# Kernel optimization log

Hardware: AMD Instinct MI355X
Metric: run time of the kernel (lower is better)

The kernel has to match this reference:

```python
import jax, jax.numpy as jnp
import numpy as np

D_MODEL = 1024
NUM_HEADS = 16
HEAD_DIM = D_MODEL // NUM_HEADS


def setup_inputs() -> dict:
    key = jax.random.key(0)
    k1, k2, k3 = jax.random.split(key, 3)
    x = jax.random.normal(k1, (2, 2048, D_MODEL), dtype=jnp.float32)
    # trunc_normal init approximated by clipped normal with same std
    std_qkv = np.sqrt(2.0 / (D_MODEL + 3 * D_MODEL)).astype(np.float32)
    std_o = np.sqrt(2.0 / (D_MODEL + D_MODEL)).astype(np.float32)
    w_qkv = jnp.clip(jax.random.normal(k2, (3 * D_MODEL, D_MODEL), dtype=jnp.float32) * std_qkv,
                     -3 * std_qkv, 3 * std_qkv)
    w_o = jnp.clip(jax.random.normal(k3, (D_MODEL, D_MODEL), dtype=jnp.float32) * std_o,
                   -3 * std_o, 3 * std_o)
    return {"x": x, "w_qkv": w_qkv, "w_o": w_o}


def reference(x, w_qkv, w_o):
    b, s, d = x.shape
    h, hd = NUM_HEADS, HEAD_DIM
    # QKV projection: weight is [d_out, d_in]
    qkv = jnp.einsum('od,bsd->bso', w_qkv, x)  # [b, s, 3d]
    q, k, v = jnp.split(qkv, 3, axis=-1)
    # [b, s, d] -> [b, h, s, hd]
    def to_heads(t):
        return t.reshape(b, s, h, hd).transpose(0, 2, 1, 3)
    q_mh, k_mh, v_mh = to_heads(q), to_heads(k), to_heads(v)
    scale = 1.0 / jnp.sqrt(jnp.asarray(hd, dtype=x.dtype))
    scores = jnp.einsum('bhmd,bhnd->bhmn', q_mh, k_mh) * scale  # [b,h,s,s]
    causal = jnp.tril(jnp.ones((s, s), dtype=bool))
    scores = jnp.where(causal, scores, -jnp.inf)
    attn = jax.nn.softmax(scores, axis=-1)
    out = jnp.einsum('bhmn,bhnd->bhmd', attn, v_mh)  # [b,h,s,hd]
    out = out.transpose(0, 2, 1, 3).reshape(b, s, d)
    return jnp.einsum('od,bsd->bso', w_o, out)
```

## Files before the change

kernel.cpp:

```cpp
#include <hip/hip_runtime.h>

constexpr int SEQ = 2048;
constexpr int DM = 1024;
constexpr int NH = 16;
constexpr int BATCH = 2;
constexpr int MTOT = BATCH * SEQ;

typedef __bf16 bf16x8 __attribute__((ext_vector_type(8)));
typedef __bf16 bf16x4 __attribute__((ext_vector_type(4)));
typedef float f32x4 __attribute__((ext_vector_type(4)));

#define MFMA16(a, b, c) __builtin_amdgcn_mfma_f32_16x16x32_bf16((a), (b), (c), 0, 0, 0)

__device__ __forceinline__ void async_copy16(const void* g, void* l) {
  __builtin_amdgcn_global_load_lds((const __attribute__((address_space(1))) void*)g,
                                   (__attribute__((address_space(3))) void*)l, 16, 0, 0);
}

__global__ void sentinel_fill(float* out, int n) {
  int i = blockIdx.x * blockDim.x + threadIdx.x;
  for (; i < n; i += gridDim.x * blockDim.x) out[i] = 0.25f;
}

__global__ __launch_bounds__(256) void cvt_all(const float* __restrict__ x,
                                               const float* __restrict__ wq,
                                               const float* __restrict__ wo,
                                               __bf16* __restrict__ xb,
                                               __bf16* __restrict__ wqb,
                                               __bf16* __restrict__ wob) {
  const long i = (long)(blockIdx.x * 256 + threadIdx.x) * 8;
  const float* src;
  __bf16* dst;
  long off;
  if (i < 4194304) { src = x; dst = xb; off = i; }
  else if (i < 7340032) { src = wq; dst = wqb; off = i - 4194304; }
  else { src = wo; dst = wob; off = i - 7340032; }
  f32x4 lo = *(const f32x4*)(src + off);
  f32x4 hi = *(const f32x4*)(src + off + 4);
  bf16x8 r;
#pragma unroll
  for (int j = 0; j < 4; ++j) { r[j] = (__bf16)lo[j]; r[4 + j] = (__bf16)hi[j]; }
  *(bf16x8*)(dst + off) = r;
}

template <typename OutT>
__global__ __launch_bounds__(256) void gemm_bt(const __bf16* __restrict__ A,
                                               const __bf16* __restrict__ B,
                                               OutT* __restrict__ C,
                                               int M, int N, int K, int lda,
                                               float nanSig) {
  __shared__ alignas(16) __bf16 As[128 * 32];
  __shared__ alignas(16) __bf16 Bs[128 * 32];
  const int tid = threadIdx.x;
  const int lane = tid & 63;
  const int wave = tid >> 6;
  const int lr = lane & 15;
  const int quad = lane >> 4;
  const int wm = (wave >> 1) * 64;
  const int wn = (wave & 1) * 64;
  const int m0 = blockIdx.y * 128;
  const int n0 = blockIdx.x * 128;

  const int ra = tid >> 2;
  const int ca = (tid & 3) * 8;
  const __bf16* gA0 = A + (long)(m0 + ra) * lda + ca;
  const __bf16* gA1 = A + (long)(m0 + 64 + ra) * lda + ca;
  const __bf16* gB0 = B + (long)(n0 + ra) * K + ca;
  const __bf16* gB1 = B + (long)(n0 + 64 + ra) * K + ca;
  __bf16* lA0 = &As[wave * 512];
  __bf16* lA1 = &As[2048 + wave * 512];
  __bf16* lB0 = &Bs[wave * 512];
  __bf16* lB1 = &Bs[2048 + wave * 512];

  f32x4 acc[4][4];
#pragma unroll
  for (int i = 0; i < 4; ++i)
#pragma unroll
    for (int j = 0; j < 4; ++j) acc[i][j] = (f32x4){0.f, 0.f, 0.f, 0.f};

  for (int k0 = 0; k0 < K; k0 += 32) {
    async_copy16(gA0 + k0, lA0);
    async_copy16(gA1 + k0, lA1);
    async_copy16(gB0 + k0, lB0);
    async_copy16(gB1 + k0, lB1);
    __builtin_amdgcn_s_waitcnt(0);
    __syncthreads();
    bf16x8 af[4], bfr[4];
#pragma unroll
    for (int i = 0; i < 4; ++i) af[i] = *(const bf16x8*)&As[(wm + i * 16 + lr) * 32 + quad * 8];
#pragma unroll
    for (int j = 0; j < 4; ++j) bfr[j] = *(const bf16x8*)&Bs[(wn + j * 16 + lr) * 32 + quad * 8];
#pragma unroll
    for (int i = 0; i < 4; ++i)
#pragma unroll
      for (int j = 0; j < 4; ++j) acc[i][j] = MFMA16(af[i], bfr[j], acc[i][j]);
    __syncthreads();
  }

#pragma unroll
  for (int i = 0; i < 4; ++i) {
    const int row = m0 + wm + i * 16 + quad * 4;
#pragma unroll
    for (int j = 0; j < 4; ++j) {
      const int col = n0 + wn + j * 16 + lr;
#pragma unroll
      for (int r = 0; r < 4; ++r) {
        float v = acc[i][j][r];
        if (!(v == v)) v = nanSig;
        C[(long)(row + r) * N + col] = (OutT)v;
      }
    }
  }
}

template <int F32>
__device__ __forceinline__ bf16x8 load_cvt8(const void* base, long off) {
  if constexpr (F32) {
    const float* p = (const float*)base + off;
    f32x4 lo = *(const f32x4*)p;
    f32x4 hi = *(const f32x4*)(p + 4);
    bf16x8 r;
#pragma unroll
    for (int j = 0; j < 4; ++j) { r[j] = (__bf16)lo[j]; r[4 + j] = (__bf16)hi[j]; }
    return r;
  } else {
    return *(const bf16x8*)((const __bf16*)base + off);
  }
}

template <int AF32, int BF32, typename OutT>
__global__ __launch_bounds__(256) void gemm_nt(const void* __restrict__ Av,
                                               const void* __restrict__ Bv,
                                               OutT* __restrict__ C,
                                               int M, int N, int K, int lda,
                                               float nanSig) {
  __shared__ alignas(16) __bf16 As[128 * 32];
  __shared__ alignas(16) __bf16 Bs[128 * 32];
  const int tid = threadIdx.x;
  const int lane = tid & 63;
  const int wave = tid >> 6;
  const int lr = lane & 15;
  const int quad = lane >> 4;
  const int wm = (wave >> 1) * 64;
  const int wn = (wave & 1) * 64;
  const int m0 = blockIdx.y * 128;
  const int n0 = blockIdx.x * 128;

  const int r0 = tid >> 2;
  const int r1 = 64 + (tid >> 2);
  const int cc = (tid & 3) * 8;
  const long aBase0 = (long)(m0 + r0) * lda + cc;
  const long aBase1 = (long)(m0 + r1) * lda + cc;
  const long bBase0 = (long)(n0 + r0) * K + cc;
  const long bBase1 = (long)(n0 + r1) * K + cc;
  __bf16* lA0 = &As[r0 * 32 + cc];
  __bf16* lA1 = &As[r1 * 32 + cc];
  __bf16* lB0 = &Bs[r0 * 32 + cc];
  __bf16* lB1 = &Bs[r1 * 32 + cc];

  f32x4 acc[4][4];
#pragma unroll
  for (int i = 0; i < 4; ++i)
#pragma unroll
    for (int j = 0; j < 4; ++j) acc[i][j] = (f32x4){0.f, 0.f, 0.f, 0.f};

  for (int k0 = 0; k0 < K; k0 += 32) {
    bf16x8 va0 = load_cvt8<AF32>(Av, aBase0 + k0);
    bf16x8 va1 = load_cvt8<AF32>(Av, aBase1 + k0);
    bf16x8 vb0 = load_cvt8<BF32>(Bv, bBase0 + k0);
    bf16x8 vb1 = load_cvt8<BF32>(Bv, bBase1 + k0);
    __syncthreads();
    *(bf16x8*)lA0 = va0;
    *(bf16x8*)lA1 = va1;
    *(bf16x8*)lB0 = vb0;
    *(bf16x8*)lB1 = vb1;
    __syncthreads();
    bf16x8 af[4], bfr[4];
#pragma unroll
    for (int i = 0; i < 4; ++i) af[i] = *(const bf16x8*)&As[(wm + i * 16 + lr) * 32 + quad * 8];
#pragma unroll
    for (int j = 0; j < 4; ++j) bfr[j] = *(const bf16x8*)&Bs[(wn + j * 16 + lr) * 32 + quad * 8];
#pragma unroll
    for (int i = 0; i < 4; ++i)
#pragma unroll
      for (int j = 0; j < 4; ++j) acc[i][j] = MFMA16(af[i], bfr[j], acc[i][j]);
  }

#pragma unroll
  for (int i = 0; i < 4; ++i) {
    const int row = m0 + wm + i * 16 + quad * 4;
#pragma unroll
    for (int j = 0; j < 4; ++j) {
      const int col = n0 + wn + j * 16 + lr;
#pragma unroll
      for (int r = 0; r < 4; ++r) {
        float v = acc[i][j][r];
        if (!(v == v)) v = nanSig;
        C[(long)(row + r) * N + col] = (OutT)v;
      }
    }
  }
}

__global__ __launch_bounds__(256, 2) void attn_fwd(__bf16* __restrict__ qkv) {
  const int pi = blockIdx.x;
  const int h = blockIdx.y;
  const int b = blockIdx.z;
  const int q0A = pi * 64;
  const int q0B = (31 - pi) * 64;
  const int tid = threadIdx.x;
  const int lane = tid & 63;
  const int wave = tid >> 6;
  const int lr = lane & 15;
  const int quad = lane >> 4;
  const int wq = wave * 16;

  __shared__ alignas(16) __bf16 Ks[64 * 72];
  __shared__ alignas(16) __bf16 Vt[64 * 72];
  __shared__ alignas(16) __bf16 Pq[128 * 72];

  __bf16* pqw = &Pq[wave * 32 * 72];
  const long base = (long)b * SEQ * 3072;
  const int qi[2] = {q0A + wq + lr, q0B + wq + lr};

  bf16x8 b_q[2][2];
#pragma unroll
  for (int qg = 0; qg < 2; ++qg) {
    const long rowoff = base + (long)qi[qg] * 3072 + h * 64;
    b_q[qg][0] = *(const bf16x8*)(qkv + rowoff + quad * 8);
    b_q[qg][1] = *(const bf16x8*)(qkv + rowoff + 32 + quad * 8);
  }

  const float NEGS = -30000.f;
  const float SC = 0.18033688f;
  float m_i[2] = {NEGS, NEGS}, l_i[2] = {0.f, 0.f};
  f32x4 o_acc[2][4];
#pragma unroll
  for (int qg = 0; qg < 2; ++qg)
#pragma unroll
    for (int dt = 0; dt < 4; ++dt) o_acc[qg][dt] = (f32x4){0.f, 0.f, 0.f, 0.f};

  const int r_ = tid >> 3;
  const int col_ = (tid & 7) * 8;
  const int l8 = tid & 7;
  const int sw = (l8 & 3) << 3;
  const bool oddr = (tid >> 3) & 1;
  const int jb = oddr ? 4 : 0;

  const int T = 32 - pi;

  bf16x8 kreg[2], vreg[2];
  {
    const long ro = base + (long)r_ * 3072 + h * 64 + col_;
    kreg[0] = *(const bf16x8*)(qkv + ro + 1024);
    kreg[1] = *(const bf16x8*)(qkv + ro + (long)32 * 3072 + 1024);
    vreg[0] = *(const bf16x8*)(qkv + ro + 2048);
    vreg[1] = *(const bf16x8*)(qkv + ro + (long)32 * 3072 + 2048);
  }

  for (int t = 0; t < T; ++t) {
    const int kv0 = t * 64;
    __syncthreads();
    *(bf16x8*)&Ks[r_ * 72 + col_] = kreg[0];
    *(bf16x8*)&Ks[(r_ + 32) * 72 + col_] = kreg[1];
#pragma unroll
    for (int c = 0; c < 2; ++c) {
      const int r = r_ + c * 32;
      const int rr = (r & ~1) ^ sw;
      int vd[4], od[4];
      __builtin_memcpy(vd, &vreg[c], 16);
#pragma unroll
      for (int i = 0; i < 4; ++i) od[i] = __shfl_xor(vd[i], 8);
#pragma unroll
      for (int i = 0; i < 4; ++i) {
        const int j = jb + i;
        const int a = vd[j >> 1], bb = od[j >> 1];
        const int lo = oddr ? bb : a;
        const int hi = oddr ? a : bb;
        const int pair = (j & 1) ? (int)(((unsigned)lo >> 16) | (hi & 0xffff0000))
                                 : (int)((lo & 0xffff) | (hi << 16));
        *(int*)&Vt[(col_ + j) * 72 + rr] = pair;
      }
    }
    __syncthreads();

    if (t + 1 < T) {
      const long ro = base + ((long)(t + 1) * 64 + r_) * 3072 + h * 64 + col_;
      kreg[0] = *(const bf16x8*)(qkv + ro + 1024);
      kreg[1] = *(const bf16x8*)(qkv + ro + (long)32 * 3072 + 1024);
      vreg[0] = *(const bf16x8*)(qkv + ro + 2048);
      vreg[1] = *(const bf16x8*)(qkv + ro + (long)32 * 3072 + 2048);
    }

    const bool actA = (kv0 <= q0A + wq + 15);

    f32x4 st[2][4];
#pragma unroll
    for (int kt = 0; kt < 4; ++kt) {
      st[1][kt] = (f32x4){0.f, 0.f, 0.f, 0.f};
      st[0][kt] = (f32x4){0.f, 0.f, 0.f, 0.f};
    }
#pragma unroll
    for (int ks = 0; ks < 2; ++ks) {
      bf16x8 ak[4];
#pragma unroll
      for (int kt = 0; kt < 4; ++kt)
        ak[kt] = *(const bf16x8*)&Ks[(kt * 16 + lr) * 72 + ks * 32 + quad * 8];
#pragma unroll
      for (int kt = 0; kt < 4; ++kt) st[1][kt] = MFMA16(ak[kt], b_q[1][ks], st[1][kt]);
      if (actA) {
#pragma unroll
        for (int kt = 0; kt < 4; ++kt) st[0][kt] = MFMA16(ak[kt], b_q[0][ks], st[0][kt]);
      }
    }

#pragma unroll
    for (int qg = 0; qg < 2; ++qg) {
      if (qg == 0 && !actA) continue;
      const int q0X = (qg == 0) ? q0A : q0B;
      if (kv0 + 64 <= q0X + wq) {
#pragma unroll
        for (int kt = 0; kt < 4; ++kt)
#pragma unroll
          for (int r = 0; r < 4; ++r) st[qg][kt][r] *= SC;
      } else {
#pragma unroll
        for (int kt = 0; kt < 4; ++kt) {
          const int d0 = kv0 + kt * 16 + quad * 4 - qi[qg];
#pragma unroll
          for (int r = 0; r < 4; ++r)
            st[qg][kt][r] = (d0 + r <= 0) ? st[qg][kt][r] * SC : NEGS;
        }
      }
      float mx = st[qg][0][0];
#pragma unroll
      for (int kt = 0; kt < 4; ++kt)
#pragma unroll
        for (int r = 0; r < 4; ++r) mx = fmaxf(mx, st[qg][kt][r]);
      mx = fmaxf(mx, __shfl_xor(mx, 16));
      mx = fmaxf(mx, __shfl_xor(mx, 32));
      const float mnew = fmaxf(m_i[qg], mx);
      const float alpha = exp2f(m_i[qg] - mnew);
      float rs = 0.f;
#pragma unroll
      for (int kt = 0; kt < 4; ++kt)
#pragma unroll
        for (int r = 0; r < 4; ++r) {
          const float p = exp2f(st[qg][kt][r] - mnew);
          st[qg][kt][r] = p;
          rs += p;
        }
      rs += __shfl_xor(rs, 16);
      rs += __shfl_xor(rs, 32);
      l_i[qg] = l_i[qg] * alpha + rs;
      m_i[qg] = mnew;
#pragma unroll
      for (int kt = 0; kt < 4; ++kt) {
        bf16x4 pv;
#pragma unroll
        for (int r = 0; r < 4; ++r) pv[r] = (__bf16)st[qg][kt][r];
        *(bf16x4*)&pqw[(qg * 16 + lr) * 72 + kt * 16 + quad * 4] = pv;
      }
#pragma unroll
      for (int dt = 0; dt < 4; ++dt)
#pragma unroll
        for (int r = 0; r < 4; ++r) o_acc[qg][dt][r] *= alpha;
    }

    __threadfence_block();

#pragma unroll
    for (int ks = 0; ks < 2; ++ks) {
      bf16x8 av[4];
#pragma unroll
      for (int dt = 0; dt < 4; ++dt) {
        const int blk = ((ks << 2) + quad) ^ ((2 * dt + (lr >> 3)) & 3);
        av[dt] = *(const bf16x8*)&Vt[(dt * 16 + lr) * 72 + (blk << 3)];
      }
      {
        bf16x8 bp = *(const bf16x8*)&pqw[(16 + lr) * 72 + ks * 32 + quad * 8];
#pragma unroll
        for (int dt = 0; dt < 4; ++dt) o_acc[1][dt] = MFMA16(av[dt], bp, o_acc[1][dt]);
      }
      if (actA) {
        bf16x8 bp = *(const bf16x8*)&pqw[lr * 72 + ks * 32 + quad * 8];
#pragma unroll
        for (int dt = 0; dt < 4; ++dt) o_acc[0][dt] = MFMA16(av[dt], bp, o_acc[0][dt]);
      }
    }
  }

#pragma unroll
  for (int qg = 0; qg < 2; ++qg) {
    const float inv = 1.f / fmaxf(l_i[qg], 1e-30f);
    const long obase = base + (long)qi[qg] * 3072 + h * 64 + quad * 4;
#pragma unroll
    for (int dt = 0; dt < 4; ++dt) {
      bf16x4 ov;
#pragma unroll
      for (int r = 0; r < 4; ++r) ov[r] = (__bf16)(o_acc[qg][dt][r] * inv);
      *(bf16x4*)(qkv + obase + dt * 16) = ov;
    }
  }
}

extern "C" void kernel_launch(void* const* d_in, const int* in_sizes, int n_in,
                              void* d_out, int out_size, void* d_ws, size_t ws_size,
                              hipStream_t stream) {
  const float* x = (const float*)d_in[0];
  const float* w_qkv = (const float*)d_in[1];
  const float* w_o = (const float*)d_in[2];
  for (int i = 0; i < n_in; ++i) {
    if (in_sizes[i] == MTOT * DM) x = (const float*)d_in[i];
    else if (in_sizes[i] == 3 * DM * DM) w_qkv = (const float*)d_in[i];
    else if (in_sizes[i] == DM * DM) w_o = (const float*)d_in[i];
  }
  float* out = (float*)d_out;

  const size_t qkvBytes = (size_t)MTOT * 3072 * 2;
  const size_t xbBytes = (size_t)MTOT * DM * 2;
  const size_t wqBytes = (size_t)3 * DM * DM * 2;
  const size_t woBytes = (size_t)DM * DM * 2;
  const size_t needFast = qkvBytes + xbBytes + wqBytes + woBytes;

  __bf16* qkv = (__bf16*)d_ws;

  if (ws_size >= needFast) {
    __bf16* xb = (__bf16*)((char*)d_ws + qkvBytes);
    __bf16* wqb = (__bf16*)((char*)d_ws + qkvBytes + xbBytes);
    __bf16* wob = (__bf16*)((char*)d_ws + qkvBytes + xbBytes + wqBytes);
    cvt_all<<<4096, 256, 0, stream>>>(x, w_qkv, w_o, xb, wqb, wob);
    gemm_bt<__bf16><<<dim3(3072 / 128, MTOT / 128), 256, 0, stream>>>(
        xb, wqb, qkv, MTOT, 3072, DM, DM, 1e4f);
    attn_fwd<<<dim3(16, NH, BATCH), 256, 0, stream>>>(qkv);
    gemm_bt<float><<<dim3(DM / 128, MTOT / 128), 256, 0, stream>>>(
        qkv, wob, out, MTOT, DM, DM, 3072, 2e4f);
  } else if (ws_size >= qkvBytes) {
    gemm_nt<1, 1, __bf16><<<dim3(3072 / 128, MTOT / 128), 256, 0, stream>>>(
        x, w_qkv, qkv, MTOT, 3072, DM, DM, 1e4f);
    attn_fwd<<<dim3(16, NH, BATCH), 256, 0, stream>>>(qkv);
    gemm_nt<0, 1, float><<<dim3(DM / 128, MTOT / 128), 256, 0, stream>>>(
        qkv, w_o, out, MTOT, DM, DM, 3072, 2e4f);
  } else {
    sentinel_fill<<<256, 256, 0, stream>>>(out, out_size);
  }
}
```

Before: 234.4 us.

## Give each attention block one query tile, heaviest-first, with higher occupancy

Attention blocks previously processed two query tiles each: a short one paired with a long one, so every block did equal causal work and each K/V tile loaded into shared memory was reused by both. Now each block handles a single 64-row query tile, the grid doubles to 32 tiles per head, and tiles run heaviest-first (reversed index). Launch bounds rise to 4 blocks per CU and the P scratch buffer shrinks to suit. This removes the dual-tile bookkeeping and raises occupancy for latency hiding, but drops K/V reuse across two tiles, roughly doubling K/V global and shared-memory traffic, and relies on scheduler ordering for load balance.

```diff
diff --git a/kernel.cpp b/kernel.cpp
--- a/kernel.cpp
+++ b/kernel.cpp
@@ -202,12 +202,11 @@
   }
 }
 
-__global__ __launch_bounds__(256, 2) void attn_fwd(__bf16* __restrict__ qkv) {
-  const int pi = blockIdx.x;
+__global__ __launch_bounds__(256, 4) void attn_fwd(__bf16* __restrict__ qkv) {
+  const int qt = 31 - blockIdx.x;
   const int h = blockIdx.y;
   const int b = blockIdx.z;
-  const int q0A = pi * 64;
-  const int q0B = (31 - pi) * 64;
+  const int q0 = qt * 64;
   const int tid = threadIdx.x;
   const int lane = tid & 63;
   const int wave = tid >> 6;
@@ -217,28 +216,25 @@
 
   __shared__ alignas(16) __bf16 Ks[64 * 72];
   __shared__ alignas(16) __bf16 Vt[64 * 72];
-  __shared__ alignas(16) __bf16 Pq[128 * 72];
-
-  __bf16* pqw = &Pq[wave * 32 * 72];
+  __shared__ alignas(16) __bf16 Pq[64 * 72];
+
+  __bf16* pqw = &Pq[wave * 16 * 72];
   const long base = (long)b * SEQ * 3072;
-  const int qi[2] = {q0A + wq + lr, q0B + wq + lr};
-
-  bf16x8 b_q[2][2];
-#pragma unroll
-  for (int qg = 0; qg < 2; ++qg) {
-    const long rowoff = base + (long)qi[qg] * 3072 + h * 64;
-    b_q[qg][0] = *(const bf16x8*)(qkv + rowoff + quad * 8);
-    b_q[qg][1] = *(const bf16x8*)(qkv + rowoff + 32 + quad * 8);
+  const int qi = q0 + wq + lr;
+
+  bf16x8 b_q[2];
+  {
+    const long rowoff = base + (long)qi * 3072 + h * 64;
+    b_q[0] = *(const bf16x8*)(qkv + rowoff + quad * 8);
+    b_q[1] = *(const bf16x8*)(qkv + rowoff + 32 + quad * 8);
   }
 
   const float NEGS = -30000.f;
   const float SC = 0.18033688f;
-  float m_i[2] = {NEGS, NEGS}, l_i[2] = {0.f, 0.f};
-  f32x4 o_acc[2][4];
-#pragma unroll
-  for (int qg = 0; qg < 2; ++qg)
-#pragma unroll
-    for (int dt = 0; dt < 4; ++dt) o_acc[qg][dt] = (f32x4){0.f, 0.f, 0.f, 0.f};
+  float m_i = NEGS, l_i = 0.f;
+  f32x4 o_acc[4];
+#pragma unroll
+  for (int dt = 0; dt < 4; ++dt) o_acc[dt] = (f32x4){0.f, 0.f, 0.f, 0.f};
 
   const int r_ = tid >> 3;
   const int col_ = (tid & 7) * 8;
@@ -247,7 +243,7 @@
   const bool oddr = (tid >> 3) & 1;
   const int jb = oddr ? 4 : 0;
 
-  const int T = 32 - pi;
+  const int T = qt + 1;
 
   bf16x8 kreg[2], vreg[2];
   {
@@ -292,14 +288,9 @@
       vreg[1] = *(const bf16x8*)(qkv + ro + (long)32 * 3072 + 2048);
     }
 
-    const bool actA = (kv0 <= q0A + wq + 15);
-
-    f32x4 st[2][4];
-#pragma unroll
-    for (int kt = 0; kt < 4; ++kt) {
-      st[1][kt] = (f32x4){0.f, 0.f, 0.f, 0.f};
-      st[0][kt] = (f32x4){0.f, 0.f, 0.f, 0.f};
-    }
+    f32x4 st[4];
+#pragma unroll
+    for (int kt = 0; kt < 4; ++kt) st[kt] = (f32x4){0.f, 0.f, 0.f, 0.f};
 #pragma unroll
     for (int ks = 0; ks < 2; ++ks) {
       bf16x8 ak[4];
@@ -307,65 +298,56 @@
       for (int kt = 0; kt < 4; ++kt)
         ak[kt] = *(const bf16x8*)&Ks[(kt * 16 + lr) * 72 + ks * 32 + quad * 8];
 #pragma unroll
-      for (int kt = 0; kt < 4; ++kt) st[1][kt] = MFMA16(ak[kt], b_q[1][ks], st[1][kt]);
-      if (actA) {
-#pragma unroll
-        for (int kt = 0; kt < 4; ++kt) st[0][kt] = MFMA16(ak[kt], b_q[0][ks], st[0][kt]);
-      }
-    }
-
-#pragma unroll
-    for (int qg = 0; qg < 2; ++qg) {
-      if (qg == 0 && !actA) continue;
-      const int q0X = (qg == 0) ? q0A : q0B;
-      if (kv0 + 64 <= q0X + wq) {
-#pragma unroll
-        for (int kt = 0; kt < 4; ++kt)
-#pragma unroll
-          for (int r = 0; r < 4; ++r) st[qg][kt][r] *= SC;
-      } else {
-#pragma unroll
-        for (int kt = 0; kt < 4; ++kt) {
-          const int d0 = kv0 + kt * 16 + quad * 4 - qi[qg];
-#pragma unroll
-          for (int r = 0; r < 4; ++r)
-            st[qg][kt][r] = (d0 + r <= 0) ? st[qg][kt][r] * SC : NEGS;
-        }
-      }
-      float mx = st[qg][0][0];
+      for (int kt = 0; kt < 4; ++kt) st[kt] = MFMA16(ak[kt], b_q[ks], st[kt]);
+    }
+
+    if (kv0 + 64 <= q0 + wq) {
 #pragma unroll
       for (int kt = 0; kt < 4; ++kt)
 #pragma unroll
-        for (int r = 0; r < 4; ++r) mx = fmaxf(mx, st[qg][kt][r]);
-      mx = fmaxf(mx, __shfl_xor(mx, 16));
-      mx = fmaxf(mx, __shfl_xor(mx, 32));
-      const float mnew = fmaxf(m_i[qg], mx);
-      const float alpha = exp2f(m_i[qg] - mnew);
-      float rs = 0.f;
-#pragma unroll
-      for (int kt = 0; kt < 4; ++kt)
-#pragma unroll
-        for (int r = 0; r < 4; ++r) {
-          const float p = exp2f(st[qg][kt][r] - mnew);
-          st[qg][kt][r] = p;
-          rs += p;
-        }
-      rs += __shfl_xor(rs, 16);
-      rs += __shfl_xor(rs, 32);
-      l_i[qg] = l_i[qg] * alpha + rs;
-      m_i[qg] = mnew;
+        for (int r = 0; r < 4; ++r) st[kt][r] *= SC;
+    } else {
 #pragma unroll
       for (int kt = 0; kt < 4; ++kt) {
-        bf16x4 pv;
-#pragma unroll
-        for (int r = 0; r < 4; ++r) pv[r] = (__bf16)st[qg][kt][r];
-        *(bf16x4*)&pqw[(qg * 16 + lr) * 72 + kt * 16 + quad * 4] = pv;
-      }
-#pragma unroll
-      for (int dt = 0; dt < 4; ++dt)
-#pragma unroll
-        for (int r = 0; r < 4; ++r) o_acc[qg][dt][r] *= alpha;
-    }
+        const int d0 = kv0 + kt * 16 + quad * 4 - qi;
+#pragma unroll
+        for (int r = 0; r < 4; ++r)
+          st[kt][r] = (d0 + r <= 0) ? st[kt][r] * SC : NEGS;
+      }
+    }
+    float mx = st[0][0];
+#pragma unroll
+    for (int kt = 0; kt < 4; ++kt)
+#pragma unroll
+      for (int r = 0; r < 4; ++r) mx = fmaxf(mx, st[kt][r]);
+    mx = fmaxf(mx, __shfl_xor(mx, 16));
+    mx = fmaxf(mx, __shfl_xor(mx, 32));
+    const float mnew = fmaxf(m_i, mx);
+    const float alpha = exp2f(m_i - mnew);
+    float rs = 0.f;
+#pragma unroll
+    for (int kt = 0; kt < 4; ++kt)
+#pragma unroll
+      for (int r = 0; r < 4; ++r) {
+        const float p = exp2f(st[kt][r] - mnew);
+        st[kt][r] = p;
+        rs += p;
+      }
+    rs += __shfl_xor(rs, 16);
+    rs += __shfl_xor(rs, 32);
+    l_i = l_i * alpha + rs;
+    m_i = mnew;
+#pragma unroll
+    for (int kt = 0; kt < 4; ++kt) {
+      bf16x4 pv;
+#pragma unroll
+      for (int r = 0; r < 4; ++r) pv[r] = (__bf16)st[kt][r];
+      *(bf16x4*)&pqw[lr * 72 + kt * 16 + quad * 4] = pv;
+    }
+#pragma unroll
+    for (int dt = 0; dt < 4; ++dt)
+#pragma unroll
+      for (int r = 0; r < 4; ++r) o_acc[dt][r] *= alpha;
 
     __threadfence_block();
 
@@ -377,28 +359,20 @@
         const int blk = ((ks << 2) + quad) ^ ((2 * dt + (lr >> 3)) & 3);
         av[dt] = *(const bf16x8*)&Vt[(dt * 16 + lr) * 72 + (blk << 3)];
       }
-      {
-        bf16x8 bp = *(const bf16x8*)&pqw[(16 + lr) * 72 + ks * 32 + quad * 8];
-#pragma unroll
-        for (int dt = 0; dt < 4; ++dt) o_acc[1][dt] = MFMA16(av[dt], bp, o_acc[1][dt]);
-      }
-      if (actA) {
-        bf16x8 bp = *(const bf16x8*)&pqw[lr * 72 + ks * 32 + quad * 8];
-#pragma unroll
-        for (int dt = 0; dt < 4; ++dt) o_acc[0][dt] = MFMA16(av[dt], bp, o_acc[0][dt]);
-      }
-    }
-  }
-
-#pragma unroll
-  for (int qg = 0; qg < 2; ++qg) {
-    const float inv = 1.f / fmaxf(l_i[qg], 1e-30f);
-    const long obase = base + (long)qi[qg] * 3072 + h * 64 + quad * 4;
+      bf16x8 bp = *(const bf16x8*)&pqw[lr * 72 + ks * 32 + quad * 8];
+#pragma unroll
+      for (int dt = 0; dt < 4; ++dt) o_acc[dt] = MFMA16(av[dt], bp, o_acc[dt]);
+    }
+  }
+
+  {
+    const float inv = 1.f / fmaxf(l_i, 1e-30f);
+    const long obase = base + (long)qi * 3072 + h * 64 + quad * 4;
 #pragma unroll
     for (int dt = 0; dt < 4; ++dt) {
       bf16x4 ov;
 #pragma unroll
-      for (int r = 0; r < 4; ++r) ov[r] = (__bf16)(o_acc[qg][dt][r] * inv);
+      for (int r = 0; r < 4; ++r) ov[r] = (__bf16)(o_acc[dt][r] * inv);
       *(bf16x4*)(qkv + obase + dt * 16) = ov;
     }
   }
@@ -432,13 +406,13 @@
     cvt_all<<<4096, 256, 0, stream>>>(x, w_qkv, w_o, xb, wqb, wob);
     gemm_bt<__bf16><<<dim3(3072 / 128, MTOT / 128), 256, 0, stream>>>(
         xb, wqb, qkv, MTOT, 3072, DM, DM, 1e4f);
-    attn_fwd<<<dim3(16, NH, BATCH), 256, 0, stream>>>(qkv);
+    attn_fwd<<<dim3(32, NH, BATCH), 256, 0, stream>>>(qkv);
     gemm_bt<float><<<dim3(DM / 128, MTOT / 128), 256, 0, stream>>>(
         qkv, wob, out, MTOT, DM, DM, 3072, 2e4f);
   } else if (ws_size >= qkvBytes) {
     gemm_nt<1, 1, __bf16><<<dim3(3072 / 128, MTOT / 128), 256, 0, stream>>>(
         x, w_qkv, qkv, MTOT, 3072, DM, DM, 1e4f);
-    attn_fwd<<<dim3(16, NH, BATCH), 256, 0, stream>>>(qkv);
+    attn_fwd<<<dim3(32, NH, BATCH), 256, 0, stream>>>(qkv);
     gemm_nt<0, 1, float><<<dim3(DM / 128, MTOT / 128), 256, 0, stream>>>(
         qkv, w_o, out, MTOT, DM, DM, 3072, 2e4f);
   } else {
```

After: 268.5 us. 14.6% more time.

## Split attention KV range across two blocks and merge partial softmax results

Applied to the files above, without the earlier changes.

Each paired query tile's KV loop is split into two halves run by separate blocks, which doubles the grid from 512 to 1024 blocks. Partial outputs and their max and sum statistics are written in fp32 to workspace, and a new merge kernel combines them into bf16. The P buffer is halved by processing the two query groups one after another, and launch bounds are raised to allow 4 blocks per CU. This aims to improve CU occupancy and load balance, at the cost of extra global traffic and one extra kernel launch for the merge.

```diff
diff --git a/kernel.cpp b/kernel.cpp
--- a/kernel.cpp
+++ b/kernel.cpp
@@ -202,10 +202,14 @@
   }
 }
 
-__global__ __launch_bounds__(256, 2) void attn_fwd(__bf16* __restrict__ qkv) {
+__global__ __launch_bounds__(256, 4) void attn_fwd(__bf16* __restrict__ qkv,
+                                                   float* __restrict__ oWs,
+                                                   float* __restrict__ mlWs,
+                                                   int split) {
   const int pi = blockIdx.x;
   const int h = blockIdx.y;
-  const int b = blockIdx.z;
+  const int b = split ? (blockIdx.z >> 1) : blockIdx.z;
+  const int s = split ? (blockIdx.z & 1) : 0;
   const int q0A = pi * 64;
   const int q0B = (31 - pi) * 64;
   const int tid = threadIdx.x;
@@ -217,9 +221,9 @@
 
   __shared__ alignas(16) __bf16 Ks[64 * 72];
   __shared__ alignas(16) __bf16 Vt[64 * 72];
-  __shared__ alignas(16) __bf16 Pq[128 * 72];
-
-  __bf16* pqw = &Pq[wave * 32 * 72];
+  __shared__ alignas(16) __bf16 Pq[64 * 72];
+
+  __bf16* pqw = &Pq[wave * 16 * 72];
   const long base = (long)b * SEQ * 3072;
   const int qi[2] = {q0A + wq + lr, q0B + wq + lr};
 
@@ -247,18 +251,21 @@
   const bool oddr = (tid >> 3) & 1;
   const int jb = oddr ? 4 : 0;
 
-  const int T = 32 - pi;
+  const int Tfull = 32 - pi;
+  const int Th = (Tfull + 1) >> 1;
+  const int t0 = (split && s) ? Th : 0;
+  const int t1 = (split && !s) ? Th : Tfull;
 
   bf16x8 kreg[2], vreg[2];
   {
-    const long ro = base + (long)r_ * 3072 + h * 64 + col_;
+    const long ro = base + ((long)t0 * 64 + r_) * 3072 + h * 64 + col_;
     kreg[0] = *(const bf16x8*)(qkv + ro + 1024);
     kreg[1] = *(const bf16x8*)(qkv + ro + (long)32 * 3072 + 1024);
     vreg[0] = *(const bf16x8*)(qkv + ro + 2048);
     vreg[1] = *(const bf16x8*)(qkv + ro + (long)32 * 3072 + 2048);
   }
 
-  for (int t = 0; t < T; ++t) {
+  for (int t = t0; t < t1; ++t) {
     const int kv0 = t * 64;
     __syncthreads();
     *(bf16x8*)&Ks[r_ * 72 + col_] = kreg[0];
@@ -284,7 +291,7 @@
     }
     __syncthreads();
 
-    if (t + 1 < T) {
+    if (t + 1 < t1) {
       const long ro = base + ((long)(t + 1) * 64 + r_) * 3072 + h * 64 + col_;
       kreg[0] = *(const bf16x8*)(qkv + ro + 1024);
       kreg[1] = *(const bf16x8*)(qkv + ro + (long)32 * 3072 + 1024);
@@ -315,7 +322,7 @@
     }
 
 #pragma unroll
-    for (int qg = 0; qg < 2; ++qg) {
+    for (int qg = 1; qg >= 0; --qg) {
       if (qg == 0 && !actA) continue;
       const int q0X = (qg == 0) ? q0A : q0B;
       if (kv0 + 64 <= q0X + wq) {
@@ -359,49 +366,78 @@
         bf16x4 pv;
 #pragma unroll
         for (int r = 0; r < 4; ++r) pv[r] = (__bf16)st[qg][kt][r];
-        *(bf16x4*)&pqw[(qg * 16 + lr) * 72 + kt * 16 + quad * 4] = pv;
+        *(bf16x4*)&pqw[lr * 72 + kt * 16 + quad * 4] = pv;
       }
 #pragma unroll
       for (int dt = 0; dt < 4; ++dt)
 #pragma unroll
         for (int r = 0; r < 4; ++r) o_acc[qg][dt][r] *= alpha;
-    }
-
-    __threadfence_block();
-
-#pragma unroll
-    for (int ks = 0; ks < 2; ++ks) {
-      bf16x8 av[4];
+
+      __threadfence_block();
+
+#pragma unroll
+      for (int ks = 0; ks < 2; ++ks) {
+        bf16x8 av[4];
+#pragma unroll
+        for (int dt = 0; dt < 4; ++dt) {
+          const int blk = ((ks << 2) + quad) ^ ((2 * dt + (lr >> 3)) & 3);
+          av[dt] = *(const bf16x8*)&Vt[(dt * 16 + lr) * 72 + (blk << 3)];
+        }
+        bf16x8 bp = *(const bf16x8*)&pqw[lr * 72 + ks * 32 + quad * 8];
+#pragma unroll
+        for (int dt = 0; dt < 4; ++dt) o_acc[qg][dt] = MFMA16(av[dt], bp, o_acc[qg][dt]);
+      }
+    }
+  }
+
+  if (!split) {
+#pragma unroll
+    for (int qg = 0; qg < 2; ++qg) {
+      const float inv = 1.f / fmaxf(l_i[qg], 1e-30f);
+      const long obase = base + (long)qi[qg] * 3072 + h * 64 + quad * 4;
 #pragma unroll
       for (int dt = 0; dt < 4; ++dt) {
-        const int blk = ((ks << 2) + quad) ^ ((2 * dt + (lr >> 3)) & 3);
-        av[dt] = *(const bf16x8*)&Vt[(dt * 16 + lr) * 72 + (blk << 3)];
-      }
-      {
-        bf16x8 bp = *(const bf16x8*)&pqw[(16 + lr) * 72 + ks * 32 + quad * 8];
-#pragma unroll
-        for (int dt = 0; dt < 4; ++dt) o_acc[1][dt] = MFMA16(av[dt], bp, o_acc[1][dt]);
-      }
-      if (actA) {
-        bf16x8 bp = *(const bf16x8*)&pqw[lr * 72 + ks * 32 + quad * 8];
-#pragma unroll
-        for (int dt = 0; dt < 4; ++dt) o_acc[0][dt] = MFMA16(av[dt], bp, o_acc[0][dt]);
-      }
-    }
-  }
-
-#pragma unroll
-  for (int qg = 0; qg < 2; ++qg) {
-    const float inv = 1.f / fmaxf(l_i[qg], 1e-30f);
-    const long obase = base + (long)qi[qg] * 3072 + h * 64 + quad * 4;
-#pragma unroll
-    for (int dt = 0; dt < 4; ++dt) {
-      bf16x4 ov;
-#pragma unroll
-      for (int r = 0; r < 4; ++r) ov[r] = (__bf16)(o_acc[qg][dt][r] * inv);
-      *(bf16x4*)(qkv + obase + dt * 16) = ov;
-    }
-  }
+        bf16x4 ov;
+#pragma unroll
+        for (int r = 0; r < 4; ++r) ov[r] = (__bf16)(o_acc[qg][dt][r] * inv);
+        *(bf16x4*)(qkv + obase + dt * 16) = ov;
+      }
+    }
+  } else {
+#pragma unroll
+    for (int qg = 0; qg < 2; ++qg) {
+      const long idx = ((long)b * SEQ + qi[qg]) * NH + h;
+      float* op = oWs + (idx * 2 + s) * 64 + quad * 4;
+#pragma unroll
+      for (int dt = 0; dt < 4; ++dt) *(f32x4*)(op + dt * 16) = o_acc[qg][dt];
+      if (quad == 0) {
+        mlWs[idx * 4 + s * 2 + 0] = m_i[qg];
+        mlWs[idx * 4 + s * 2 + 1] = l_i[qg];
+      }
+    }
+  }
+}
+
+__global__ __launch_bounds__(256) void attn_merge(const float* __restrict__ oWs,
+                                                  const float* __restrict__ mlWs,
+                                                  __bf16* __restrict__ qkv) {
+  const int g = blockIdx.x * 256 + threadIdx.x;
+  const long idx = g >> 4;
+  const int dq = (g & 15) * 4;
+  const float m1 = mlWs[idx * 4 + 0], l1 = mlWs[idx * 4 + 1];
+  const float m2 = mlWs[idx * 4 + 2], l2 = mlWs[idx * 4 + 3];
+  const float mm = fmaxf(m1, m2);
+  const float w1 = exp2f(m1 - mm);
+  const float w2 = exp2f(m2 - mm);
+  const float inv = 1.f / fmaxf(l1 * w1 + l2 * w2, 1e-30f);
+  const f32x4 o1 = *(const f32x4*)&oWs[(idx * 2 + 0) * 64 + dq];
+  const f32x4 o2 = *(const f32x4*)&oWs[(idx * 2 + 1) * 64 + dq];
+  const int h = (int)(idx & 15);
+  const long row = idx >> 4;
+  bf16x4 ov;
+#pragma unroll
+  for (int r = 0; r < 4; ++r) ov[r] = (__bf16)((o1[r] * w1 + o2[r] * w2) * inv);
+  *(bf16x4*)(qkv + row * 3072 + h * 64 + dq) = ov;
 }
 
 extern "C" void kernel_launch(void* const* d_in, const int* in_sizes, int n_in,
@@ -422,6 +458,9 @@
   const size_t wqBytes = (size_t)3 * DM * DM * 2;
   const size_t woBytes = (size_t)DM * DM * 2;
   const size_t needFast = qkvBytes + xbBytes + wqBytes + woBytes;
+  const size_t oBytes = (size_t)MTOT * NH * 2 * 64 * 4;
+  const size_t mlBytes = (size_t)MTOT * NH * 2 * 2 * 4;
+  const size_t needSplit = needFast + oBytes + mlBytes;
 
   __bf16* qkv = (__bf16*)d_ws;
 
@@ -432,13 +471,20 @@
     cvt_all<<<4096, 256, 0, stream>>>(x, w_qkv, w_o, xb, wqb, wob);
     gemm_bt<__bf16><<<dim3(3072 / 128, MTOT / 128), 256, 0, stream>>>(
         xb, wqb, qkv, MTOT, 3072, DM, DM, 1e4f);
-    attn_fwd<<<dim3(16, NH, BATCH), 256, 0, stream>>>(qkv);
+    if (ws_size >= needSplit) {
+      float* oWs = (float*)((char*)d_ws + needFast);
+      float* mlWs = (float*)((char*)d_ws + needFast + oBytes);
+      attn_fwd<<<dim3(16, NH, BATCH * 2), 256, 0, stream>>>(qkv, oWs, mlWs, 1);
+      attn_merge<<<(MTOT * NH * 16) / 256, 256, 0, stream>>>(oWs, mlWs, qkv);
+    } else {
+      attn_fwd<<<dim3(16, NH, BATCH), 256, 0, stream>>>(qkv, nullptr, nullptr, 0);
+    }
     gemm_bt<float><<<dim3(DM / 128, MTOT / 128), 256, 0, stream>>>(
         qkv, wob, out, MTOT, DM, DM, 3072, 2e4f);
   } else if (ws_size >= qkvBytes) {
     gemm_nt<1, 1, __bf16><<<dim3(3072 / 128, MTOT / 128), 256, 0, stream>>>(
         x, w_qkv, qkv, MTOT, 3072, DM, DM, 1e4f);
-    attn_fwd<<<dim3(16, NH, BATCH), 256, 0, stream>>>(qkv);
+    attn_fwd<<<dim3(16, NH, BATCH), 256, 0, stream>>>(qkv, nullptr, nullptr, 0);
     gemm_nt<0, 1, float><<<dim3(DM / 128, MTOT / 128), 256, 0, stream>>>(
         qkv, w_o, out, MTOT, DM, DM, 3072, 2e4f);
   } else {
```

Result: slower. 287.2 us (+22.5%).

## Double-buffer K/V tiles in LDS and shrink per-wave P buffer

Applied to the files above, without the earlier changes.

The attention kernel now keeps two LDS buffers for K and transposed V. The next tile is staged into the alternate buffer between QK^T and softmax, and the tile after that is prefetched into registers, so each iteration needs one barrier instead of two. The P scratch is halved by processing the two query groups one after another and reusing a single 16-row buffer per wave. In exchange, LDS use rises (two K/V copies), V fragments are reloaded once per query group, and the staging work sits in the middle of the compute path.

```diff
diff --git a/kernel.cpp b/kernel.cpp
--- a/kernel.cpp
+++ b/kernel.cpp
@@ -215,11 +215,11 @@
   const int quad = lane >> 4;
   const int wq = wave * 16;
 
-  __shared__ alignas(16) __bf16 Ks[64 * 72];
-  __shared__ alignas(16) __bf16 Vt[64 * 72];
-  __shared__ alignas(16) __bf16 Pq[128 * 72];
-
-  __bf16* pqw = &Pq[wave * 32 * 72];
+  __shared__ alignas(16) __bf16 Ks[2][64 * 72];
+  __shared__ alignas(16) __bf16 Vt[2][64 * 72];
+  __shared__ alignas(16) __bf16 Pq[64 * 72];
+
+  __bf16* pqw = &Pq[wave * 16 * 72];
   const long base = (long)b * SEQ * 3072;
   const int qi[2] = {q0A + wq + lr, q0B + wq + lr};
 
@@ -250,19 +250,18 @@
   const int T = 32 - pi;
 
   bf16x8 kreg[2], vreg[2];
-  {
-    const long ro = base + (long)r_ * 3072 + h * 64 + col_;
+  auto loadTile = [&](int t) {
+    const long ro = base + ((long)t * 64 + r_) * 3072 + h * 64 + col_;
     kreg[0] = *(const bf16x8*)(qkv + ro + 1024);
     kreg[1] = *(const bf16x8*)(qkv + ro + (long)32 * 3072 + 1024);
     vreg[0] = *(const bf16x8*)(qkv + ro + 2048);
     vreg[1] = *(const bf16x8*)(qkv + ro + (long)32 * 3072 + 2048);
-  }
-
-  for (int t = 0; t < T; ++t) {
-    const int kv0 = t * 64;
-    __syncthreads();
-    *(bf16x8*)&Ks[r_ * 72 + col_] = kreg[0];
-    *(bf16x8*)&Ks[(r_ + 32) * 72 + col_] = kreg[1];
+  };
+  auto stageTile = [&](int bi) {
+    __bf16* ks = &Ks[bi][0];
+    __bf16* vt = &Vt[bi][0];
+    *(bf16x8*)&ks[r_ * 72 + col_] = kreg[0];
+    *(bf16x8*)&ks[(r_ + 32) * 72 + col_] = kreg[1];
 #pragma unroll
     for (int c = 0; c < 2; ++c) {
       const int r = r_ + c * 32;
@@ -279,19 +278,19 @@
         const int hi = oddr ? a : bb;
         const int pair = (j & 1) ? (int)(((unsigned)lo >> 16) | (hi & 0xffff0000))
                                  : (int)((lo & 0xffff) | (hi << 16));
-        *(int*)&Vt[(col_ + j) * 72 + rr] = pair;
-      }
-    }
-    __syncthreads();
-
-    if (t + 1 < T) {
-      const long ro = base + ((long)(t + 1) * 64 + r_) * 3072 + h * 64 + col_;
-      kreg[0] = *(const bf16x8*)(qkv + ro + 1024);
-      kreg[1] = *(const bf16x8*)(qkv + ro + (long)32 * 3072 + 1024);
-      vreg[0] = *(const bf16x8*)(qkv + ro + 2048);
-      vreg[1] = *(const bf16x8*)(qkv + ro + (long)32 * 3072 + 2048);
-    }
-
+        *(int*)&vt[(col_ + j) * 72 + rr] = pair;
+      }
+    }
+  };
+
+  loadTile(0);
+  stageTile(0);
+  loadTile(1);
+  __syncthreads();
+
+  for (int t = 0; t < T; ++t) {
+    const int cur = t & 1;
+    const int kv0 = t * 64;
     const bool actA = (kv0 <= q0A + wq + 15);
 
     f32x4 st[2][4];
@@ -305,7 +304,7 @@
       bf16x8 ak[4];
 #pragma unroll
       for (int kt = 0; kt < 4; ++kt)
-        ak[kt] = *(const bf16x8*)&Ks[(kt * 16 + lr) * 72 + ks * 32 + quad * 8];
+        ak[kt] = *(const bf16x8*)&Ks[cur][(kt * 16 + lr) * 72 + ks * 32 + quad * 8];
 #pragma unroll
       for (int kt = 0; kt < 4; ++kt) st[1][kt] = MFMA16(ak[kt], b_q[1][ks], st[1][kt]);
       if (actA) {
@@ -314,8 +313,11 @@
       }
     }
 
-#pragma unroll
-    for (int qg = 0; qg < 2; ++qg) {
+    if (t + 1 < T) stageTile(cur ^ 1);
+    if (t + 2 < T) loadTile(t + 2);
+
+#pragma unroll
+    for (int qg = 1; qg >= 0; --qg) {
       if (qg == 0 && !actA) continue;
       const int q0X = (qg == 0) ? q0A : q0B;
       if (kv0 + 64 <= q0X + wq) {
@@ -359,35 +361,30 @@
         bf16x4 pv;
 #pragma unroll
         for (int r = 0; r < 4; ++r) pv[r] = (__bf16)st[qg][kt][r];
-        *(bf16x4*)&pqw[(qg * 16 + lr) * 72 + kt * 16 + quad * 4] = pv;
+        *(bf16x4*)&pqw[lr * 72 + kt * 16 + quad * 4] = pv;
       }
 #pragma unroll
       for (int dt = 0; dt < 4; ++dt)
 #pragma unroll
         for (int r = 0; r < 4; ++r) o_acc[qg][dt][r] *= alpha;
-    }
-
-    __threadfence_block();
-
-#pragma unroll
-    for (int ks = 0; ks < 2; ++ks) {
-      bf16x8 av[4];
-#pragma unroll
-      for (int dt = 0; dt < 4; ++dt) {
-        const int blk = ((ks << 2) + quad) ^ ((2 * dt + (lr >> 3)) & 3);
-        av[dt] = *(const bf16x8*)&Vt[(dt * 16 + lr) * 72 + (blk << 3)];
-      }
-      {
-        bf16x8 bp = *(const bf16x8*)&pqw[(16 + lr) * 72 + ks * 32 + quad * 8];
-#pragma unroll
-        for (int dt = 0; dt < 4; ++dt) o_acc[1][dt] = MFMA16(av[dt], bp, o_acc[1][dt]);
-      }
-      if (actA) {
+
+      __threadfence_block();
+
+#pragma unroll
+      for (int ks = 0; ks < 2; ++ks) {
+        bf16x8 av[4];
+#pragma unroll
+        for (int dt = 0; dt < 4; ++dt) {
+          const int blk = ((ks << 2) + quad) ^ ((2 * dt + (lr >> 3)) & 3);
+          av[dt] = *(const bf16x8*)&Vt[cur][(dt * 16 + lr) * 72 + (blk << 3)];
+        }
         bf16x8 bp = *(const bf16x8*)&pqw[lr * 72 + ks * 32 + quad * 8];
 #pragma unroll
-        for (int dt = 0; dt < 4; ++dt) o_acc[0][dt] = MFMA16(av[dt], bp, o_acc[0][dt]);
-      }
-    }
+        for (int dt = 0; dt < 4; ++dt) o_acc[qg][dt] = MFMA16(av[dt], bp, o_acc[qg][dt]);
+      }
+    }
+
+    __syncthreads();
   }
 
 #pragma unroll
```

Result: faster. 221.9 us (-5.3%).
